# Performance work log

Measured on AMD Instinct MI355X. Metric: run time of the kernel, lower is better.

The kernel has to match this reference:

```python
import jax, jax.numpy as jnp
import numpy as np

BETA = 0.25


def setup_inputs() -> dict:
    key = jax.random.key(0)
    k1, k2 = jax.random.split(key)
    ze = jax.random.normal(k1, (16, 64, 64, 64), dtype=jnp.float32)  # (B, L, H, W)
    # codebook init mirrors uniform_(-1/K, 1/K)
    K = 1024
    emb = jax.random.uniform(k2, (K, 64), dtype=jnp.float32, minval=-1.0 / K, maxval=1.0 / K)
    return {"ze": ze, "emb": emb}


def reference(ze, emb):
    B, L, H, W = ze.shape
    K = emb.shape[0]
    # (B, H, W, L) -> (N, L)
    zf = jnp.transpose(ze, (0, 2, 3, 1)).reshape(-1, L)
    # squared euclidean distances (N, K)
    d = (jnp.sum(zf * zf, axis=1, keepdims=True)
         + jnp.sum(emb * emb, axis=1)
         - 2.0 * zf @ emb.T)
    idx = jnp.argmin(d, axis=1)  # (N,)
    # direct gather == one-hot @ emb
    z_q = jnp.transpose(emb[idx].reshape(B, H, W, L), (0, 3, 1, 2))
    loss = (jnp.mean((jax.lax.stop_gradient(z_q) - ze) ** 2)
            + BETA * jnp.mean((z_q - jax.lax.stop_gradient(ze)) ** 2))
    # straight-through estimator
    z_q_st = ze + jax.lax.stop_gradient(z_q - ze)
    # perplexity of code usage
    counts = jnp.zeros((K,), dtype=zf.dtype).at[idx].add(1.0)
    e_mean = counts / zf.shape[0]
    perplexity = jnp.exp(-jnp.sum(e_mean * jnp.log(e_mean + 1e-10)))
    return z_q_st, loss, idx.reshape(-1, 1)
```

## Files before the change

### kernel.cpp

```cpp
#include <hip/hip_runtime.h>

typedef short bf16x8 __attribute__((ext_vector_type(8)));
typedef float f32x4  __attribute__((ext_vector_type(4)));

#define CAP 12

#define WS_LOSS 0
#define WS_DONE 8
#define WS_EBF  64

#define L_EBF   0
#define L_MARG  131072
#define L_CCNT  132096
#define L_CSLOT 133120
#define L_TOTAL 145408

__device__ __forceinline__ unsigned short f2bf(float f) {
    unsigned u = __float_as_uint(f);
    return (unsigned short)((u + 0x7fffu + ((u >> 16) & 1u)) >> 16);
}

__device__ __forceinline__ float np_pairwise_sumsq64(const float* a) {
    float r[8];
    #pragma unroll
    for (int j = 0; j < 8; ++j) r[j] = __fmul_rn(a[j], a[j]);
    #pragma unroll
    for (int i = 8; i < 64; i += 8)
        #pragma unroll
        for (int j = 0; j < 8; ++j)
            r[j] = __fadd_rn(r[j], __fmul_rn(a[i + j], a[i + j]));
    return __fadd_rn(
        __fadd_rn(__fadd_rn(r[0], r[1]), __fadd_rn(r[2], r[3])),
        __fadd_rn(__fadd_rn(r[4], r[5]), __fadd_rn(r[6], r[7])));
}

__global__ __launch_bounds__(256) void prep_kernel(
    const float* __restrict__ emb, unsigned short* __restrict__ ebf,
    float* __restrict__ loss, int* __restrict__ done)
{
    int k = blockIdx.x * 256 + threadIdx.x;
    if (k == 0) { *loss = 0.0f; *done = 0; }
    if (k < 1024) {
        float e[64];
        #pragma unroll
        for (int l = 0; l < 64; ++l) e[l] = emb[k * 64 + l];
        int tile = k >> 4, r = k & 15;
        #pragma unroll
        for (int j = 0; j < 8; ++j) {
            bf16x8 v;
            #pragma unroll
            for (int m = 0; m < 8; ++m) v[m] = (short)f2bf(e[j * 8 + m]);
            *(bf16x8*)(ebf + tile * 1024 + j * 128 + r * 8) = v;
        }
    }
}

__global__ __launch_bounds__(256)
__attribute__((amdgpu_waves_per_eu(1, 1)))
void vq_kernel(
    const float* __restrict__ ze, const float* __restrict__ emb,
    const unsigned short* __restrict__ ebf,
    float* __restrict__ out_zq, float* __restrict__ out_idxf,
    float* __restrict__ loss, int* __restrict__ done,
    float* __restrict__ out_loss)
{
    extern __shared__ char smem[];
    unsigned short* ebf_l  = (unsigned short*)(smem + L_EBF);
    unsigned short* zbf    = (unsigned short*)(smem + L_EBF);
    float*          marg_l = (float*)(smem + L_MARG);
    int*            ccnt   = (int*)(smem + L_CCNT);
    int*            cslot  = (int*)(smem + L_CSLOT);

    const int t = threadIdx.x;
    const int n0 = blockIdx.x * 256;
    const int gbase = (n0 >> 12) * 262144 + (n0 & 4095);

    float z[64];
    {
        const float* zp = ze + gbase + t;
        #pragma unroll
        for (int l = 0; l < 64; ++l) z[l] = zp[l * 4096];
    }
    ccnt[t] = 0;
    const float znorm = np_pairwise_sumsq64(z);
    {
        float S = 0.0f;
        #pragma unroll
        for (int l = 0; l < 64; ++l) S += fabsf(z[l]);
        marg_l[t] = 1.67e-5f * S + 2.0e-4f;
    }
    {
        const int swt = t & 7;
        #pragma unroll
        for (int c = 0; c < 8; ++c) {
            bf16x8 bv;
            #pragma unroll
            for (int m = 0; m < 8; ++m) bv[m] = (short)f2bf(z[c * 8 + m]);
            *(bf16x8*)&zbf[t * 64 + ((c ^ swt) * 8)] = bv;
        }
    }
    __syncthreads();

    const int wv = t >> 6, lane = t & 63;
    const int r = lane & 15, q = lane >> 4;
    const int wp = wv * 64;
    const int sw = r & 7;
    bf16x8 a0[4], a1[4];
    #pragma unroll
    for (int rg = 0; rg < 4; ++rg) {
        int pg = wp + rg * 16 + r;
        a0[rg] = *(bf16x8*)&zbf[pg * 64 + ((q ^ sw) * 8)];
        a1[rg] = *(bf16x8*)&zbf[pg * 64 + (((q + 4) ^ sw) * 8)];
    }
    __syncthreads();

    {
        const bf16x8* src = (const bf16x8*)ebf;
        bf16x8* dst = (bf16x8*)ebf_l;
        #pragma unroll 8
        for (int i = 0; i < 32; ++i) dst[t + i * 256] = src[t + i * 256];
    }
    __syncthreads();

    const unsigned short* bptr = ebf_l + q * 128 + r * 8;

    float rm[16];
    #pragma unroll
    for (int i = 0; i < 16; ++i) rm[i] = -1e30f;
    {
        bf16x8 pb0[2], pb1[2];
        pb0[0] = *(const bf16x8*)(bptr);
        pb1[0] = *(const bf16x8*)(bptr + 512);
        pb0[1] = *(const bf16x8*)(bptr + 1024);
        pb1[1] = *(const bf16x8*)(bptr + 1536);
        #pragma unroll 4
        for (int tile = 0; tile < 64; ++tile) {
            bf16x8 b0 = pb0[tile & 1], b1 = pb1[tile & 1];
            int nt = tile + 2; if (nt > 63) nt = 63;
            pb0[tile & 1] = *(const bf16x8*)(bptr + nt * 1024);
            pb1[tile & 1] = *(const bf16x8*)(bptr + nt * 1024 + 512);
            #pragma unroll
            for (int rg = 0; rg < 4; ++rg) {
                f32x4 c = {0.f, 0.f, 0.f, 0.f};
                c = __builtin_amdgcn_mfma_f32_16x16x32_bf16(a0[rg], b0, c, 0, 0, 0);
                c = __builtin_amdgcn_mfma_f32_16x16x32_bf16(a1[rg], b1, c, 0, 0, 0);
                #pragma unroll
                for (int i = 0; i < 4; ++i)
                    rm[rg * 4 + i] = fmaxf(rm[rg * 4 + i], c[i]);
            }
        }
    }
    float thr[16];
    #pragma unroll
    for (int j = 0; j < 16; ++j) {
        float v = rm[j];
        v = fmaxf(v, __shfl_xor(v, 1, 16));
        v = fmaxf(v, __shfl_xor(v, 2, 16));
        v = fmaxf(v, __shfl_xor(v, 4, 16));
        v = fmaxf(v, __shfl_xor(v, 8, 16));
        int row = wp + (j >> 2) * 16 + q * 4 + (j & 3);
        thr[j] = v - 0.5f * marg_l[row];
    }

    {
        bf16x8 pb0[2], pb1[2];
        pb0[0] = *(const bf16x8*)(bptr);
        pb1[0] = *(const bf16x8*)(bptr + 512);
        pb0[1] = *(const bf16x8*)(bptr + 1024);
        pb1[1] = *(const bf16x8*)(bptr + 1536);
        #pragma unroll 4
        for (int tile = 0; tile < 64; ++tile) {
            bf16x8 b0 = pb0[tile & 1], b1 = pb1[tile & 1];
            int nt = tile + 2; if (nt > 63) nt = 63;
            pb0[tile & 1] = *(const bf16x8*)(bptr + nt * 1024);
            pb1[tile & 1] = *(const bf16x8*)(bptr + nt * 1024 + 512);
            int code = tile * 16 + r;
            #pragma unroll
            for (int rg = 0; rg < 4; ++rg) {
                f32x4 c = {0.f, 0.f, 0.f, 0.f};
                c = __builtin_amdgcn_mfma_f32_16x16x32_bf16(a0[rg], b0, c, 0, 0, 0);
                c = __builtin_amdgcn_mfma_f32_16x16x32_bf16(a1[rg], b1, c, 0, 0, 0);
                #pragma unroll
                for (int i = 0; i < 4; ++i) {
                    if (c[i] >= thr[rg * 4 + i]) {
                        int pp = wp + rg * 16 + q * 4 + i;
                        int ci = atomicAdd(&ccnt[pp], 1);
                        if (ci < CAP) cslot[pp * CAP + ci] = code;
                    }
                }
            }
        }
    }
    __syncthreads();

    int cnt = ccnt[t]; if (cnt > CAP) cnt = CAP;
    float best = 1e30f; int bk = 1 << 20;
    for (int c = 0; c < cnt; ++c) {
        int k = cslot[t * CAP + c];
        float e[64];
        const float4* er = (const float4*)(emb + k * 64);
        #pragma unroll
        for (int j = 0; j < 16; ++j) {
            float4 v = er[j];
            e[4*j] = v.x; e[4*j+1] = v.y; e[4*j+2] = v.z; e[4*j+3] = v.w;
        }
        float en = np_pairwise_sumsq64(e);
        float acc = 0.0f;
        #pragma unroll
        for (int l = 0; l < 64; ++l) acc = fmaf(z[l], e[l], acc);
        float sc = __fsub_rn(__fadd_rn(znorm, en), __fmul_rn(2.0f, acc));
        if (sc < best || (sc == best && k < bk)) { best = sc; bk = k; }
    }
    out_idxf[n0 + t] = (float)bk;

    {
        const float4* er = (const float4*)(emb + bk * 64);
        float ls = 0.0f;
        #pragma unroll
        for (int j = 0; j < 16; ++j) {
            float4 v = er[j];
            float vv[4] = {v.x, v.y, v.z, v.w};
            #pragma unroll
            for (int m = 0; m < 4; ++m) {
                int l = 4 * j + m;
                out_zq[gbase + t + l * 4096] = vv[m];
                float d = vv[m] - z[l];
                ls = fmaf(d, d, ls);
            }
        }
        #pragma unroll
        for (int off = 32; off > 0; off >>= 1) ls += __shfl_down(ls, off, 64);
        if (lane == 0) atomicAdd(loss, ls);
    }

    __syncthreads();
    if (t == 0) {
        __threadfence();
        int old = atomicAdd(done, 1);
        if (old == (int)gridDim.x - 1) {
            __threadfence();
            float total = atomicAdd(loss, 0.0f);
            *out_loss = 1.25f * total / 4194304.0f;
        }
    }
}

extern "C" void kernel_launch(void* const* d_in, const int* in_sizes, int n_in,
                              void* d_out, int out_size, void* d_ws, size_t ws_size,
                              hipStream_t stream)
{
    const float* ze  = (const float*)d_in[0];
    const float* emb = (const float*)d_in[1];
    float* out = (float*)d_out;
    float* out_zq   = out;
    float* out_loss = out + 4194304;
    float* out_idxf = out + 4194305;

    char* w = (char*)d_ws;
    float*          ws_loss = (float*)(w + WS_LOSS);
    int*            ws_done = (int*)(w + WS_DONE);
    unsigned short* ebf     = (unsigned short*)(w + WS_EBF);

    static bool attr_set = false;
    if (!attr_set) {
        hipFuncSetAttribute((const void*)vq_kernel,
                            hipFuncAttributeMaxDynamicSharedMemorySize, L_TOTAL);
        attr_set = true;
    }

    prep_kernel<<<4, 256, 0, stream>>>(emb, ebf, ws_loss, ws_done);
    vq_kernel<<<256, 256, L_TOTAL, stream>>>(ze, emb, ebf, out_zq, out_idxf,
                                             ws_loss, ws_done, out_loss);
}
```

Before: 141.5 us.

## Double threads per block by splitting codebook halves across wave groups

The block grows from 256 to 512 threads. Two groups of four waves each scan half of the codebook in the MFMA passes, and their per-row maxima are merged through shared memory before thresholding. The first half of the threads computes the margins while the second half copies the bf16 codebook into LDS, so the two phases overlap. A-fragments are now built directly from global memory instead of being staged through LDS, and the output/loss write is split over all 512 threads. This adds an extra barrier and re-reads ze from global several times, and the single-EU-wave-per-SIMD scheduling changes to two waves.

```diff
diff --git a/kernel.cpp b/kernel.cpp
--- a/kernel.cpp
+++ b/kernel.cpp
@@ -9,11 +9,13 @@
 #define WS_DONE 8
 #define WS_EBF  64
 
-#define L_EBF   0
-#define L_MARG  131072
-#define L_CCNT  132096
-#define L_CSLOT 133120
-#define L_TOTAL 145408
+#define L_EBF    0
+#define L_MARG   131072
+#define L_CCNT   132096
+#define L_KCH    133120
+#define L_ROWMAX 134144
+#define L_CSLOT  136192
+#define L_TOTAL  148480
 
 __device__ __forceinline__ unsigned short f2bf(float f) {
     unsigned u = __float_as_uint(f);
@@ -55,8 +57,8 @@
     }
 }
 
-__global__ __launch_bounds__(256)
-__attribute__((amdgpu_waves_per_eu(1, 1)))
+__global__ __launch_bounds__(512)
+__attribute__((amdgpu_waves_per_eu(2, 2)))
 void vq_kernel(
     const float* __restrict__ ze, const float* __restrict__ emb,
     const unsigned short* __restrict__ ebf,
@@ -65,64 +67,49 @@
     float* __restrict__ out_loss)
 {
     extern __shared__ char smem[];
-    unsigned short* ebf_l  = (unsigned short*)(smem + L_EBF);
-    unsigned short* zbf    = (unsigned short*)(smem + L_EBF);
-    float*          marg_l = (float*)(smem + L_MARG);
-    int*            ccnt   = (int*)(smem + L_CCNT);
-    int*            cslot  = (int*)(smem + L_CSLOT);
+    unsigned short* ebf_l   = (unsigned short*)(smem + L_EBF);
+    float*          marg_l  = (float*)(smem + L_MARG);
+    int*            ccnt    = (int*)(smem + L_CCNT);
+    int*            kch     = (int*)(smem + L_KCH);
+    float*          rowmax2 = (float*)(smem + L_ROWMAX);
+    int*            cslot   = (int*)(smem + L_CSLOT);
 
     const int t = threadIdx.x;
     const int n0 = blockIdx.x * 256;
     const int gbase = (n0 >> 12) * 262144 + (n0 & 4095);
 
-    float z[64];
-    {
+    if (t < 256) {
         const float* zp = ze + gbase + t;
-        #pragma unroll
-        for (int l = 0; l < 64; ++l) z[l] = zp[l * 4096];
-    }
-    ccnt[t] = 0;
-    const float znorm = np_pairwise_sumsq64(z);
-    {
         float S = 0.0f;
         #pragma unroll
-        for (int l = 0; l < 64; ++l) S += fabsf(z[l]);
+        for (int l = 0; l < 64; ++l) S += fabsf(zp[l * 4096]);
         marg_l[t] = 1.67e-5f * S + 2.0e-4f;
-    }
-    {
-        const int swt = t & 7;
-        #pragma unroll
-        for (int c = 0; c < 8; ++c) {
-            bf16x8 bv;
-            #pragma unroll
-            for (int m = 0; m < 8; ++m) bv[m] = (short)f2bf(z[c * 8 + m]);
-            *(bf16x8*)&zbf[t * 64 + ((c ^ swt) * 8)] = bv;
-        }
-    }
-    __syncthreads();
-
-    const int wv = t >> 6, lane = t & 63;
-    const int r = lane & 15, q = lane >> 4;
-    const int wp = wv * 64;
-    const int sw = r & 7;
-    bf16x8 a0[4], a1[4];
-    #pragma unroll
-    for (int rg = 0; rg < 4; ++rg) {
-        int pg = wp + rg * 16 + r;
-        a0[rg] = *(bf16x8*)&zbf[pg * 64 + ((q ^ sw) * 8)];
-        a1[rg] = *(bf16x8*)&zbf[pg * 64 + (((q + 4) ^ sw) * 8)];
-    }
-    __syncthreads();
-
-    {
+        ccnt[t] = 0;
+    } else {
+        const int tt = t - 256;
         const bf16x8* src = (const bf16x8*)ebf;
         bf16x8* dst = (bf16x8*)ebf_l;
         #pragma unroll 8
-        for (int i = 0; i < 32; ++i) dst[t + i * 256] = src[t + i * 256];
-    }
-    __syncthreads();
-
-    const unsigned short* bptr = ebf_l + q * 128 + r * 8;
+        for (int i = 0; i < 32; ++i) dst[tt + i * 256] = src[tt + i * 256];
+    }
+
+    const int wv = t >> 6, lane = t & 63;
+    const int r = lane & 15, q = lane >> 4;
+    const int pg = wv & 3, kh = wv >> 2;
+    const int wp = pg * 64;
+    bf16x8 a0[4], a1[4];
+    #pragma unroll
+    for (int rg = 0; rg < 4; ++rg) {
+        const float* zb = ze + gbase + wp + rg * 16 + r;
+        #pragma unroll
+        for (int j = 0; j < 8; ++j) {
+            a0[rg][j] = (short)f2bf(zb[(q * 8 + j) * 4096]);
+            a1[rg][j] = (short)f2bf(zb[(32 + q * 8 + j) * 4096]);
+        }
+    }
+    __syncthreads();
+
+    const unsigned short* bptr = ebf_l + (kh * 32) * 1024 + q * 128 + r * 8;
 
     float rm[16];
     #pragma unroll
@@ -134,9 +121,9 @@
         pb0[1] = *(const bf16x8*)(bptr + 1024);
         pb1[1] = *(const bf16x8*)(bptr + 1536);
         #pragma unroll 4
-        for (int tile = 0; tile < 64; ++tile) {
+        for (int tile = 0; tile < 32; ++tile) {
             bf16x8 b0 = pb0[tile & 1], b1 = pb1[tile & 1];
-            int nt = tile + 2; if (nt > 63) nt = 63;
+            int nt = tile + 2; if (nt > 31) nt = 31;
             pb0[tile & 1] = *(const bf16x8*)(bptr + nt * 1024);
             pb1[tile & 1] = *(const bf16x8*)(bptr + nt * 1024 + 512);
             #pragma unroll
@@ -150,7 +137,6 @@
             }
         }
     }
-    float thr[16];
     #pragma unroll
     for (int j = 0; j < 16; ++j) {
         float v = rm[j];
@@ -159,7 +145,15 @@
         v = fmaxf(v, __shfl_xor(v, 4, 16));
         v = fmaxf(v, __shfl_xor(v, 8, 16));
         int row = wp + (j >> 2) * 16 + q * 4 + (j & 3);
-        thr[j] = v - 0.5f * marg_l[row];
+        if (r == 0) rowmax2[row * 2 + kh] = v;
+    }
+    __syncthreads();
+
+    float thr[16];
+    #pragma unroll
+    for (int j = 0; j < 16; ++j) {
+        int row = wp + (j >> 2) * 16 + q * 4 + (j & 3);
+        thr[j] = fmaxf(rowmax2[row * 2], rowmax2[row * 2 + 1]) - 0.5f * marg_l[row];
     }
 
     {
@@ -169,12 +163,12 @@
         pb0[1] = *(const bf16x8*)(bptr + 1024);
         pb1[1] = *(const bf16x8*)(bptr + 1536);
         #pragma unroll 4
-        for (int tile = 0; tile < 64; ++tile) {
+        for (int tile = 0; tile < 32; ++tile) {
             bf16x8 b0 = pb0[tile & 1], b1 = pb1[tile & 1];
-            int nt = tile + 2; if (nt > 63) nt = 63;
+            int nt = tile + 2; if (nt > 31) nt = 31;
             pb0[tile & 1] = *(const bf16x8*)(bptr + nt * 1024);
             pb1[tile & 1] = *(const bf16x8*)(bptr + nt * 1024 + 512);
-            int code = tile * 16 + r;
+            int code = kh * 512 + tile * 16 + r;
             #pragma unroll
             for (int rg = 0; rg < 4; ++rg) {
                 f32x4 c = {0.f, 0.f, 0.f, 0.f};
@@ -193,40 +187,49 @@
     }
     __syncthreads();
 
-    int cnt = ccnt[t]; if (cnt > CAP) cnt = CAP;
-    float best = 1e30f; int bk = 1 << 20;
-    for (int c = 0; c < cnt; ++c) {
-        int k = cslot[t * CAP + c];
-        float e[64];
-        const float4* er = (const float4*)(emb + k * 64);
-        #pragma unroll
-        for (int j = 0; j < 16; ++j) {
-            float4 v = er[j];
-            e[4*j] = v.x; e[4*j+1] = v.y; e[4*j+2] = v.z; e[4*j+3] = v.w;
-        }
-        float en = np_pairwise_sumsq64(e);
-        float acc = 0.0f;
-        #pragma unroll
-        for (int l = 0; l < 64; ++l) acc = fmaf(z[l], e[l], acc);
-        float sc = __fsub_rn(__fadd_rn(znorm, en), __fmul_rn(2.0f, acc));
-        if (sc < best || (sc == best && k < bk)) { best = sc; bk = k; }
-    }
-    out_idxf[n0 + t] = (float)bk;
+    if (t < 256) {
+        float z[64];
+        const float* zp = ze + gbase + t;
+        #pragma unroll
+        for (int l = 0; l < 64; ++l) z[l] = zp[l * 4096];
+        float znorm = np_pairwise_sumsq64(z);
+        int cnt = ccnt[t]; if (cnt > CAP) cnt = CAP;
+        float best = 1e30f; int bk = 1 << 20;
+        for (int c = 0; c < cnt; ++c) {
+            int k = cslot[t * CAP + c];
+            float e[64];
+            const float4* er = (const float4*)(emb + k * 64);
+            #pragma unroll
+            for (int j = 0; j < 16; ++j) {
+                float4 v = er[j];
+                e[4*j] = v.x; e[4*j+1] = v.y; e[4*j+2] = v.z; e[4*j+3] = v.w;
+            }
+            float en = np_pairwise_sumsq64(e);
+            float acc = 0.0f;
+            #pragma unroll
+            for (int l = 0; l < 64; ++l) acc = fmaf(z[l], e[l], acc);
+            float sc = __fsub_rn(__fadd_rn(znorm, en), __fmul_rn(2.0f, acc));
+            if (sc < best || (sc == best && k < bk)) { best = sc; bk = k; }
+        }
+        kch[t] = bk;
+        out_idxf[n0 + t] = (float)bk;
+    }
+    __syncthreads();
 
     {
-        const float4* er = (const float4*)(emb + bk * 64);
+        const int p = t & 255, h = t >> 8;
+        const int bk = kch[p];
+        const float* er = emb + bk * 64 + h * 32;
+        const float* zp = ze + gbase + p + (h * 32) * 4096;
+        float* op = out_zq + gbase + p + (h * 32) * 4096;
         float ls = 0.0f;
         #pragma unroll
-        for (int j = 0; j < 16; ++j) {
-            float4 v = er[j];
-            float vv[4] = {v.x, v.y, v.z, v.w};
-            #pragma unroll
-            for (int m = 0; m < 4; ++m) {
-                int l = 4 * j + m;
-                out_zq[gbase + t + l * 4096] = vv[m];
-                float d = vv[m] - z[l];
-                ls = fmaf(d, d, ls);
-            }
+        for (int j = 0; j < 32; ++j) {
+            float qv = er[j];
+            float zv = zp[j * 4096];
+            op[j * 4096] = qv;
+            float d = qv - zv;
+            ls = fmaf(d, d, ls);
         }
         #pragma unroll
         for (int off = 32; off > 0; off >>= 1) ls += __shfl_down(ls, off, 64);
@@ -269,6 +272,6 @@
     }
 
     prep_kernel<<<4, 256, 0, stream>>>(emb, ebf, ws_loss, ws_done);
-    vq_kernel<<<256, 256, L_TOTAL, stream>>>(ze, emb, ebf, out_zq, out_idxf,
+    vq_kernel<<<256, 512, L_TOTAL, stream>>>(ze, emb, ebf, out_zq, out_idxf,
                                              ws_loss, ws_done, out_loss);
 }
```

Measured after the change: 139.5 us. Within noise of the previous version (-1.4%).
